# Optimization experiments

Measured on AMD Instinct MI355X. Metric: run time of the kernel, lower is better.

Reference implementation:

```python
import jax, jax.numpy as jnp
import numpy as np

LAMDA = 0.2  # config['lamda']
T, B, NI, IL, NS, H = 24, 64, 32, 24, 256, 256  # steps, batch, n_inputs, input_len(=vec), n_stations, hidden


def setup_inputs() -> dict:
    key = jax.random.key(0)
    ks = jax.random.split(key, 24)
    VEC, DIN = IL, NI + NS
    n = lambda k, s, sc=1.0: jax.random.normal(k, s, dtype=jnp.float32) * sc
    return {
        'local_inputs': n(ks[0], (T, B, NI)),
        'global_inputs': n(ks[1], (T, B, NS)),
        'local_states': n(ks[2], (B, NI, IL)),
        'global_states': n(ks[3], (B, NS, NI, IL)),
        'distmat': n(ks[4], (B, NS)),
        'local_attn0': jax.random.uniform(ks[5], (B, NI), jnp.float32, -0.25, 0.25),
        'global_attn0': jax.random.uniform(ks[6], (B, NS), jnp.float32, -0.15, 0.15),
        # conv_local_u: 1x1 conv over [B, IL, NI, 1] -> weight [VEC, IL]
        'Wcl': n(ks[7], (VEC, IL), 0.1), 'bcl': n(ks[8], (VEC,), 0.05),
        'Wll': n(ks[9], (VEC, H), 0.05), 'bll': n(ks[10], (VEC,), 0.05),
        'vl': n(ks[11], (VEC,)),
        # conv_global_k: kernel (1, NI) over [B, IL, NS, NI] -> weight [VEC, IL, NI]
        'Wcg': n(ks[12], (VEC, IL, NI), 0.05), 'bcg': n(ks[13], (VEC,), 0.05),
        'Wlg': n(ks[14], (VEC, H), 0.05), 'blg': n(ks[15], (VEC,), 0.05),
        'vg': n(ks[16], (VEC,)),
        # LSTM cell (called with zero h0/c0 every step, as in the source)
        'Wih': n(ks[17], (4 * H, DIN), 0.05),
        'bih': n(ks[18], (4 * H,), 0.05),
        'bhh': n(ks[19], (4 * H,), 0.05),
    }


def reference(local_inputs, global_inputs, local_states, global_states, distmat,
              local_attn0, global_attn0, Wcl, bcl, Wll, bll, vl,
              Wcg, bcg, Wlg, blg, vg, Wih, bih, bhh):
    b, ni, il = local_states.shape
    ns = global_states.shape[1]
    # raw .view() reshapes as in the torch code (NOT transposes)
    lhid = local_states.reshape(b, il, ni)                 # [B, IL, NI]
    hf_l = jnp.einsum('oc,bcl->bol', Wcl, lhid) + bcl[None, :, None]   # 1x1 conv
    ghid = global_states.reshape(b, il, ns, ni)            # [B, IL, NS, NI]
    hf_g = jnp.einsum('ocj,bcsj->bos', Wcg, ghid) + bcg[None, :, None]  # (1,NI) conv

    def step(carry, xs):
        la, ga = carry
        l_inp, g_inp = xs
        x = jnp.concatenate([la * l_inp, ga * g_inp], axis=1)  # [B, NI+NS]
        gates = x @ Wih.T + bih + bhh                          # h0 = 0 -> no Whh term
        i_g, f_g, g_g, o_g = jnp.split(gates, 4, axis=1)       # torch gate order i,f,g,o
        c = jax.nn.sigmoid(i_g) * jnp.tanh(g_g)                # c0 = 0 -> forget term drops
        h = jax.nn.sigmoid(o_g) * jnp.tanh(c)
        q = c                                                  # query = LSTM state
        y_l = q @ Wll.T + bll                                  # [B, VEC]
        s_l = jnp.einsum('bold,d->bl', jnp.tanh(hf_l[:, :, :, None] + y_l[:, None, None, :]), vl)
        la_n = jax.nn.softmax(s_l, axis=1)
        y_g = q @ Wlg.T + blg
        s_g = jnp.einsum('bosd,d->bs', jnp.tanh(hf_g[:, :, :, None] + y_g[:, None, None, :]), vg)
        s_g = (1.0 - LAMDA) * s_g + LAMDA * distmat
        ga_n = jax.nn.softmax(s_g, axis=1)
        return (la_n, ga_n), (h, c, la_n, ga_n)

    _, (outs, cs, las, gas) = jax.lax.scan(step, (local_attn0, global_attn0),
                                           (local_inputs, global_inputs))
    return outs, cs[-1], las, gas
```

## Files before the change

### kernel.cpp

```cpp
#include <hip/hip_runtime.h>

#define T_     24
#define LAMDA_ 0.2f

#define OFF_CS  393216
#define OFF_LAS 409600
#define OFF_GAS 458752

__device__ __forceinline__ float clamp15(float x){ return fminf(15.f, fmaxf(-15.f, x)); }
__device__ __forceinline__ float rcp_(float x){ return __builtin_amdgcn_rcpf(x); }

__global__ __launch_bounds__(1024, 4) void spat_kernel(
    const float* __restrict__ li,  const float* __restrict__ gi,
    const float* __restrict__ ls,  const float* __restrict__ gs,
    const float* __restrict__ dist,
    const float* __restrict__ la0, const float* __restrict__ ga0,
    const float* __restrict__ Wcl, const float* __restrict__ bcl,
    const float* __restrict__ Wll, const float* __restrict__ bll, const float* __restrict__ vl,
    const float* __restrict__ Wcg, const float* __restrict__ bcg,
    const float* __restrict__ Wlg, const float* __restrict__ blg, const float* __restrict__ vg,
    const float* __restrict__ Wih, const float* __restrict__ bih, const float* __restrict__ bhh,
    float* __restrict__ out)
{
    __shared__ float Eg[6144];
    __shared__ float El[800];
    __shared__ __align__(16) union {
        float wcg[6144];
        struct {
            float sgred[1024];
            float red[800];
            float gbuf[768];
            float xv[288];
            float cq[256];
        } p;
    } U;
    __shared__ float dstf[256];
    __shared__ float bsum[768];
    __shared__ float bcf[48];
    __shared__ __align__(8) float2 fvl[24], fvg[24];
    __shared__ float vlf[24], vgf[24], cbuf[2];
    __shared__ float ldspad[10240];

    const int b = blockIdx.x, tid = threadIdx.x;
    const int s = tid & 255, ogrp = tid >> 8;

    if (__builtin_expect((int)blockIdx.x == -1, 0)) {
        ldspad[tid] = bcg[0];
        out[0] = ldspad[tid ^ 1];
    }

    if (tid < 256) dstf[tid] = dist[b*256 + tid];
    if (tid < 24)  { vlf[tid] = vl[tid]; vgf[tid] = vg[tid]; }
    if (tid < 48)  bcf[tid] = (tid < 24) ? bll[tid] : blg[tid - 24];
    if (tid < 768) {
        const int wrow = tid + ((tid >= 256) ? 256 : 0);
        bsum[tid] = bih[wrow] + bhh[wrow];
    }
    if (tid == 0)  { float s1 = 0.f; for (int d = 0; d < 24; d++) s1 += vl[d]; cbuf[0] = s1; }
    if (tid == 1)  { float s1 = 0.f; for (int d = 0; d < 24; d++) s1 += vg[d]; cbuf[1] = s1; }

    float acc[6];
#pragma unroll
    for (int i = 0; i < 6; i++) acc[i] = bcg[ogrp*6 + i];

    for (int hc = 0; hc < 3; hc++) {
        for (int k = tid; k < 6144; k += 1024) {
            const int o = k >> 8, r = k & 255;
            U.wcg[k] = Wcg[o*768 + hc*256 + r];
        }
        __syncthreads();
        for (int cc = 0; cc < 8; cc++) {
            const int c = hc*8 + cc;
            const float4* gp = (const float4*)(gs + ((size_t)b*196608 + c*8192 + s*32));
#pragma unroll
            for (int h = 0; h < 2; h++) {
                float gv[16];
#pragma unroll
                for (int m = 0; m < 4; m++) {
                    const float4 g = gp[h*4 + m];
                    gv[4*m] = g.x; gv[4*m+1] = g.y; gv[4*m+2] = g.z; gv[4*m+3] = g.w;
                }
#pragma unroll
                for (int i = 0; i < 6; i++) {
                    const float4* wp = (const float4*)(U.wcg + ((ogrp*6 + i)*256 + cc*32)) + h*4;
                    float a = acc[i];
#pragma unroll
                    for (int m = 0; m < 4; m++) {
                        const float4 w = wp[m];
                        a = fmaf(w.x, gv[4*m],   a);
                        a = fmaf(w.y, gv[4*m+1], a);
                        a = fmaf(w.z, gv[4*m+2], a);
                        a = fmaf(w.w, gv[4*m+3], a);
                    }
                    acc[i] = a;
                }
            }
        }
        __syncthreads();
    }
#pragma unroll
    for (int i = 0; i < 6; i++) Eg[(ogrp*6 + i)*256 + s] = __expf(2.f*clamp15(acc[i]));

    if (tid < 768) {
        const int o = tid >> 5, l = tid & 31;
        float a = bcl[o];
        for (int c = 0; c < 24; c++)
            a = fmaf(Wcl[o*24 + c], ls[b*768 + c*32 + l], a);
        El[l*25 + o] = __expf(2.f*clamp15(a));
    }

    if (tid < 288) {
        if (tid < 32) U.p.xv[tid] = la0[b*32 + tid] * li[b*32 + tid];
        else { const int ss = tid - 32; U.p.xv[tid] = ga0[b*256 + ss] * gi[b*256 + ss]; }
    }
    __syncthreads();

    const int u8 = tid & 7, slot = tid >> 3;
    const int rbase = slot*6;

    for (int t = 0; t < T_; t++) {
        float liN = 0.f;
        float giN0 = 0.f, giN1 = 0.f, giN2 = 0.f, giN3 = 0.f;
        if (t < T_ - 1) {
            if (tid < 32) liN = li[(t+1)*2048 + b*32 + tid];
            else if (tid >= 64 && tid < 128) {
                const int lane = tid - 64;
                giN0 = gi[(t+1)*16384 + b*256 + lane];
                giN1 = gi[(t+1)*16384 + b*256 + lane + 64];
                giN2 = gi[(t+1)*16384 + b*256 + lane + 128];
                giN3 = gi[(t+1)*16384 + b*256 + lane + 192];
            }
        }

        {
            const float4* xp = (const float4*)U.p.xv;
            float ar0 = 0.f, ar1 = 0.f, ar2 = 0.f, ar3 = 0.f, ar4 = 0.f, ar5 = 0.f;
#pragma unroll 1
            for (int jc = 0; jc < 3; jc++) {
                const float4 x0 = xp[jc*24 + u8];
                const float4 x1 = xp[jc*24 + 8 + u8];
                const float4 x2 = xp[jc*24 + 16 + u8];

#define KROW(kk, AR) { \
                const int row_ = rbase + (kk); \
                const int wrow_ = row_ + ((row_ >= 256) ? 256 : 0); \
                const float4* wp_ = (const float4*)(Wih + wrow_*288) + jc*24 + u8; \
                const float4 w0_ = wp_[0], w1_ = wp_[8], w2_ = wp_[16]; \
                float a_ = AR; \
                a_ = fmaf(w0_.x,x0.x,a_); a_ = fmaf(w0_.y,x0.y,a_); \
                a_ = fmaf(w0_.z,x0.z,a_); a_ = fmaf(w0_.w,x0.w,a_); \
                a_ = fmaf(w1_.x,x1.x,a_); a_ = fmaf(w1_.y,x1.y,a_); \
                a_ = fmaf(w1_.z,x1.z,a_); a_ = fmaf(w1_.w,x1.w,a_); \
                a_ = fmaf(w2_.x,x2.x,a_); a_ = fmaf(w2_.y,x2.y,a_); \
                a_ = fmaf(w2_.z,x2.z,a_); a_ = fmaf(w2_.w,x2.w,a_); \
                AR = a_; }

                KROW(0, ar0) KROW(1, ar1)
                __builtin_amdgcn_sched_barrier(0);
                KROW(2, ar2) KROW(3, ar3)
                __builtin_amdgcn_sched_barrier(0);
                KROW(4, ar4) KROW(5, ar5)
                __builtin_amdgcn_sched_barrier(0);
#undef KROW
            }
            {
                float a_;
#define RED(kk, AR) { a_ = AR; \
                a_ += __shfl_xor(a_, 1); a_ += __shfl_xor(a_, 2); a_ += __shfl_xor(a_, 4); \
                if (u8 == 0) { const int row_ = rbase + (kk); U.p.gbuf[row_] = a_ + bsum[row_]; } }
                RED(0, ar0) RED(1, ar1) RED(2, ar2) RED(3, ar3) RED(4, ar4) RED(5, ar5)
#undef RED
            }
        }
        __syncthreads();

        if (tid < 256) {
            const float ig = U.p.gbuf[tid], gg = U.p.gbuf[256 + tid], ot = U.p.gbuf[512 + tid];
            const float sig_i = rcp_(1.f + __expf(-ig));
            const float th_g  = 1.f - 2.f*rcp_(1.f + __expf(2.f*clamp15(gg)));
            const float c     = sig_i * th_g;
            const float sig_o = rcp_(1.f + __expf(-ot));
            const float th_c  = 1.f - 2.f*rcp_(1.f + __expf(2.f*c));
            const float h     = sig_o * th_c;
            U.p.cq[tid] = c;
            out[t*16384 + b*256 + tid] = h;
            if (t == T_ - 1) out[OFF_CS + b*256 + tid] = c;
        }
        __syncthreads();

        if (tid < 384) {
            const int dot = slot;
            const float* Wr = (dot < 24) ? (Wll + dot*256) : (Wlg + (dot - 24)*256);
            const float4* wp = (const float4*)Wr;
            const float4* cp = (const float4*)U.p.cq;
            float a0 = 0.f, a1 = 0.f;
#pragma unroll
            for (int j = 0; j < 8; j += 2) {
                const float4 w0 = wp[j*8 + u8],     c0 = cp[j*8 + u8];
                const float4 w1 = wp[(j+1)*8 + u8], c1 = cp[(j+1)*8 + u8];
                a0 = fmaf(w0.x,c0.x,a0); a0 = fmaf(w0.y,c0.y,a0);
                a0 = fmaf(w0.z,c0.z,a0); a0 = fmaf(w0.w,c0.w,a0);
                a1 = fmaf(w1.x,c1.x,a1); a1 = fmaf(w1.y,c1.y,a1);
                a1 = fmaf(w1.z,c1.z,a1); a1 = fmaf(w1.w,c1.w,a1);
            }
            float a = a0 + a1;
            a += __shfl_xor(a, 1); a += __shfl_xor(a, 2); a += __shfl_xor(a, 4);
            if (u8 == 0) {
                const float F = __expf(2.f*clamp15(a + bcf[dot]));
                if (dot < 24) fvl[dot] = make_float2(F, vlf[dot]);
                else          fvg[dot - 24] = make_float2(F, vgf[dot - 24]);
            }
        }
        __syncthreads();

        {
            float Ew[6];
#pragma unroll
            for (int i = 0; i < 6; i++) Ew[i] = Eg[(ogrp*6 + i)*256 + s];
            float a0 = 0.f;
#pragma unroll
            for (int d = 0; d < 24; d++) {
                const float2 p = fvg[d];
                const float r0 = rcp_(fmaf(Ew[0], p.x, 1.f));
                const float r1 = rcp_(fmaf(Ew[1], p.x, 1.f));
                const float r2 = rcp_(fmaf(Ew[2], p.x, 1.f));
                const float r3 = rcp_(fmaf(Ew[3], p.x, 1.f));
                const float r4 = rcp_(fmaf(Ew[4], p.x, 1.f));
                const float r5 = rcp_(fmaf(Ew[5], p.x, 1.f));
                a0 = fmaf(p.y, ((r0 + r1) + (r2 + r3)) + (r4 + r5), a0);
            }
            U.p.sgred[tid] = a0;
        }
        if (tid < 768) {
            const int l = tid / 24, o = tid - l*24;
            const float E = El[l*25 + o];
            float b0 = 0.f, b1 = 0.f;
#pragma unroll
            for (int d = 0; d < 24; d += 2) {
                const float2 p0 = fvl[d], p1 = fvl[d+1];
                b0 = fmaf(p0.y, rcp_(fmaf(E, p0.x, 1.f)), b0);
                b1 = fmaf(p1.y, rcp_(fmaf(E, p1.x, 1.f)), b1);
            }
            U.p.red[l*25 + o] = b0 + b1;
        }
        __syncthreads();

        if (tid < 32) {
            float tot = 0.f;
#pragma unroll
            for (int o2 = 0; o2 < 24; o2++) tot += U.p.red[tid*25 + o2];
            const float sv = 24.f*cbuf[0] - 2.f*tot;
            float m = sv;
#pragma unroll
            for (int mk = 16; mk >= 1; mk >>= 1) m = fmaxf(m, __shfl_xor(m, mk));
            const float e = __expf(sv - m);
            float ss = e;
#pragma unroll
            for (int mk = 16; mk >= 1; mk >>= 1) ss += __shfl_xor(ss, mk);
            const float r = e * rcp_(ss);
            out[OFF_LAS + t*2048 + b*32 + tid] = r;
            if (t < T_ - 1) U.p.xv[tid] = r * liN;
        } else if (tid >= 64 && tid < 128) {
            const int lane = tid - 64;
            float vv0, vv1, vv2, vv3;
            {
                const float t0 = U.p.sgred[lane]     + U.p.sgred[256+lane]     + U.p.sgred[512+lane]     + U.p.sgred[768+lane];
                const float t1 = U.p.sgred[lane+64]  + U.p.sgred[256+lane+64]  + U.p.sgred[512+lane+64]  + U.p.sgred[768+lane+64];
                const float t2 = U.p.sgred[lane+128] + U.p.sgred[256+lane+128] + U.p.sgred[512+lane+128] + U.p.sgred[768+lane+128];
                const float t3 = U.p.sgred[lane+192] + U.p.sgred[256+lane+192] + U.p.sgred[512+lane+192] + U.p.sgred[768+lane+192];
                vv0 = (1.f-LAMDA_)*(24.f*cbuf[1] - 2.f*t0) + LAMDA_*dstf[lane];
                vv1 = (1.f-LAMDA_)*(24.f*cbuf[1] - 2.f*t1) + LAMDA_*dstf[lane+64];
                vv2 = (1.f-LAMDA_)*(24.f*cbuf[1] - 2.f*t2) + LAMDA_*dstf[lane+128];
                vv3 = (1.f-LAMDA_)*(24.f*cbuf[1] - 2.f*t3) + LAMDA_*dstf[lane+192];
            }
            float m = fmaxf(fmaxf(vv0, vv1), fmaxf(vv2, vv3));
#pragma unroll
            for (int mk = 32; mk >= 1; mk >>= 1) m = fmaxf(m, __shfl_xor(m, mk));
            const float e0 = __expf(vv0 - m), e1 = __expf(vv1 - m);
            const float e2 = __expf(vv2 - m), e3 = __expf(vv3 - m);
            float ss = (e0 + e1) + (e2 + e3);
#pragma unroll
            for (int mk = 32; mk >= 1; mk >>= 1) ss += __shfl_xor(ss, mk);
            const float inv = rcp_(ss);
            const float r0 = e0*inv, r1 = e1*inv, r2 = e2*inv, r3 = e3*inv;
            float* og = out + OFF_GAS + t*16384 + b*256;
            og[lane] = r0; og[lane+64] = r1; og[lane+128] = r2; og[lane+192] = r3;
            if (t < T_ - 1) {
                U.p.xv[32+lane]     = r0 * giN0;
                U.p.xv[32+lane+64]  = r1 * giN1;
                U.p.xv[32+lane+128] = r2 * giN2;
                U.p.xv[32+lane+192] = r3 * giN3;
            }
        }
        __syncthreads();
    }
}

extern "C" void kernel_launch(void* const* d_in, const int* in_sizes, int n_in,
                              void* d_out, int out_size, void* d_ws, size_t ws_size,
                              hipStream_t stream)
{
    const float* li   = (const float*)d_in[0];
    const float* gi   = (const float*)d_in[1];
    const float* ls   = (const float*)d_in[2];
    const float* gs   = (const float*)d_in[3];
    const float* dist = (const float*)d_in[4];
    const float* la0  = (const float*)d_in[5];
    const float* ga0  = (const float*)d_in[6];
    const float* Wcl  = (const float*)d_in[7];
    const float* bcl  = (const float*)d_in[8];
    const float* Wll  = (const float*)d_in[9];
    const float* bll  = (const float*)d_in[10];
    const float* vl   = (const float*)d_in[11];
    const float* Wcg  = (const float*)d_in[12];
    const float* bcg  = (const float*)d_in[13];
    const float* Wlg  = (const float*)d_in[14];
    const float* blg  = (const float*)d_in[15];
    const float* vg   = (const float*)d_in[16];
    const float* Wih  = (const float*)d_in[17];
    const float* bih  = (const float*)d_in[18];
    const float* bhh  = (const float*)d_in[19];

    spat_kernel<<<64, 1024, 0, stream>>>(li, gi, ls, gs, dist, la0, ga0,
                                         Wcl, bcl, Wll, bll, vl,
                                         Wcg, bcg, Wlg, blg, vg,
                                         Wih, bih, bhh, (float*)d_out);
}
```

Baseline: 542.5 us.

## Pair attention terms into rational form and buffer outputs in shared memory

Adjacent vector dimensions of the tanh-sum attention score are combined algebraically into one rational function per pair, with numerator and denominator coefficients precomputed. This halves the number of reciprocal operations in both the global and local attention loops. The local attention reduction now uses wave shuffles instead of a shared-memory array plus a serial sum. Per-step global output stores are buffered in shared memory and written out once after the time loop, and the padding LDS array is removed. Pairing changes rounding slightly and could lose precision when the E·F products are large.

```diff
diff --git a/kernel.cpp b/kernel.cpp
--- a/kernel.cpp
+++ b/kernel.cpp
@@ -24,30 +24,28 @@
 {
     __shared__ float Eg[6144];
     __shared__ float El[800];
+    __shared__ float outb[6144];
+    __shared__ float gasb[6144];
+    __shared__ float lasb[768];
+    __shared__ float csb[256];
     __shared__ __align__(16) union {
         float wcg[6144];
         struct {
             float sgred[1024];
-            float red[800];
             float gbuf[768];
             float xv[288];
             float cq[256];
+            float slg[32];
         } p;
     } U;
     __shared__ float dstf[256];
     __shared__ float bsum[768];
     __shared__ float bcf[48];
-    __shared__ __align__(8) float2 fvl[24], fvg[24];
+    __shared__ __align__(16) float4 pl4[12], pg4[12];
     __shared__ float vlf[24], vgf[24], cbuf[2];
-    __shared__ float ldspad[10240];
 
     const int b = blockIdx.x, tid = threadIdx.x;
     const int s = tid & 255, ogrp = tid >> 8;
-
-    if (__builtin_expect((int)blockIdx.x == -1, 0)) {
-        ldspad[tid] = bcg[0];
-        out[0] = ldspad[tid ^ 1];
-    }
 
     if (tid < 256) dstf[tid] = dist[b*256 + tid];
     if (tid < 24)  { vlf[tid] = vl[tid]; vgf[tid] = vg[tid]; }
@@ -117,6 +115,7 @@
 
     const int u8 = tid & 7, slot = tid >> 3;
     const int rbase = slot*6;
+    const int lg = tid >> 5, ol = tid & 31;
 
     for (int t = 0; t < T_; t++) {
         float liN = 0.f;
@@ -155,11 +154,9 @@
                 a_ = fmaf(w2_.z,x2.z,a_); a_ = fmaf(w2_.w,x2.w,a_); \
                 AR = a_; }
 
-                KROW(0, ar0) KROW(1, ar1)
+                KROW(0, ar0) KROW(1, ar1) KROW(2, ar2)
                 __builtin_amdgcn_sched_barrier(0);
-                KROW(2, ar2) KROW(3, ar3)
-                __builtin_amdgcn_sched_barrier(0);
-                KROW(4, ar4) KROW(5, ar5)
+                KROW(3, ar3) KROW(4, ar4) KROW(5, ar5)
                 __builtin_amdgcn_sched_barrier(0);
 #undef KROW
             }
@@ -183,8 +180,8 @@
             const float th_c  = 1.f - 2.f*rcp_(1.f + __expf(2.f*c));
             const float h     = sig_o * th_c;
             U.p.cq[tid] = c;
-            out[t*16384 + b*256 + tid] = h;
-            if (t == T_ - 1) out[OFF_CS + b*256 + tid] = c;
+            outb[t*256 + tid] = h;
+            if (t == T_ - 1) csb[tid] = c;
         }
         __syncthreads();
 
@@ -205,51 +202,64 @@
             }
             float a = a0 + a1;
             a += __shfl_xor(a, 1); a += __shfl_xor(a, 2); a += __shfl_xor(a, 4);
-            if (u8 == 0) {
-                const float F = __expf(2.f*clamp15(a + bcf[dot]));
-                if (dot < 24) fvl[dot] = make_float2(F, vlf[dot]);
-                else          fvg[dot - 24] = make_float2(F, vgf[dot - 24]);
+            const float F  = __expf(2.f*clamp15(a + bcf[dot]));
+            const float v  = (dot < 24) ? vlf[dot] : vgf[dot - 24];
+            const float Fo = __shfl_xor(F, 8);
+            const float vo = (dot < 24) ? vlf[dot ^ 1] : vgf[(dot ^ 1) - 24];
+            if ((tid & 15) == 0) {
+                const float A0 = v + vo;
+                const float A1 = fmaf(v, Fo, vo * F);
+                const float B1 = F + Fo;
+                const float B2 = F * Fo;
+                const int P = slot >> 1;
+                if (P < 12) pl4[P]      = make_float4(A0, A1, B1, B2);
+                else        pg4[P - 12] = make_float4(A0, A1, B1, B2);
             }
         }
         __syncthreads();
 
         {
-            float Ew[6];
-#pragma unroll
-            for (int i = 0; i < 6; i++) Ew[i] = Eg[(ogrp*6 + i)*256 + s];
+            float z[6], z2[6];
+#pragma unroll
+            for (int i = 0; i < 6; i++) {
+                z[i]  = Eg[(ogrp*6 + i)*256 + s];
+                z2[i] = z[i]*z[i];
+            }
             float a0 = 0.f;
-#pragma unroll
-            for (int d = 0; d < 24; d++) {
-                const float2 p = fvg[d];
-                const float r0 = rcp_(fmaf(Ew[0], p.x, 1.f));
-                const float r1 = rcp_(fmaf(Ew[1], p.x, 1.f));
-                const float r2 = rcp_(fmaf(Ew[2], p.x, 1.f));
-                const float r3 = rcp_(fmaf(Ew[3], p.x, 1.f));
-                const float r4 = rcp_(fmaf(Ew[4], p.x, 1.f));
-                const float r5 = rcp_(fmaf(Ew[5], p.x, 1.f));
-                a0 = fmaf(p.y, ((r0 + r1) + (r2 + r3)) + (r4 + r5), a0);
+#pragma unroll 4
+            for (int p = 0; p < 12; p++) {
+                const float4 q = pg4[p];
+#pragma unroll
+                for (int i = 0; i < 6; i++) {
+                    const float num = fmaf(z[i],  q.y, q.x);
+                    const float den = fmaf(z2[i], q.w, fmaf(z[i], q.z, 1.f));
+                    a0 = fmaf(num, rcp_(den), a0);
+                }
             }
             U.p.sgred[tid] = a0;
         }
-        if (tid < 768) {
-            const int l = tid / 24, o = tid - l*24;
-            const float E = El[l*25 + o];
-            float b0 = 0.f, b1 = 0.f;
-#pragma unroll
-            for (int d = 0; d < 24; d += 2) {
-                const float2 p0 = fvl[d], p1 = fvl[d+1];
-                b0 = fmaf(p0.y, rcp_(fmaf(E, p0.x, 1.f)), b0);
-                b1 = fmaf(p1.y, rcp_(fmaf(E, p1.x, 1.f)), b1);
-            }
-            U.p.red[l*25 + o] = b0 + b1;
+        {
+            float bsl = 0.f;
+            if (ol < 24) {
+                const float E  = El[lg*25 + ol];
+                const float E2 = E*E;
+#pragma unroll 4
+                for (int p = 0; p < 12; p++) {
+                    const float4 q = pl4[p];
+                    const float num = fmaf(E,  q.y, q.x);
+                    const float den = fmaf(E2, q.w, fmaf(E, q.z, 1.f));
+                    bsl = fmaf(num, rcp_(den), bsl);
+                }
+            }
+            bsl += __shfl_xor(bsl, 1);  bsl += __shfl_xor(bsl, 2);
+            bsl += __shfl_xor(bsl, 4);  bsl += __shfl_xor(bsl, 8);
+            bsl += __shfl_xor(bsl, 16);
+            if (ol == 0) U.p.slg[lg] = bsl;
         }
         __syncthreads();
 
         if (tid < 32) {
-            float tot = 0.f;
-#pragma unroll
-            for (int o2 = 0; o2 < 24; o2++) tot += U.p.red[tid*25 + o2];
-            const float sv = 24.f*cbuf[0] - 2.f*tot;
+            const float sv = 24.f*cbuf[0] - 2.f*U.p.slg[tid];
             float m = sv;
 #pragma unroll
             for (int mk = 16; mk >= 1; mk >>= 1) m = fmaxf(m, __shfl_xor(m, mk));
@@ -258,7 +268,7 @@
 #pragma unroll
             for (int mk = 16; mk >= 1; mk >>= 1) ss += __shfl_xor(ss, mk);
             const float r = e * rcp_(ss);
-            out[OFF_LAS + t*2048 + b*32 + tid] = r;
+            lasb[t*32 + tid] = r;
             if (t < T_ - 1) U.p.xv[tid] = r * liN;
         } else if (tid >= 64 && tid < 128) {
             const int lane = tid - 64;
@@ -283,8 +293,8 @@
             for (int mk = 32; mk >= 1; mk >>= 1) ss += __shfl_xor(ss, mk);
             const float inv = rcp_(ss);
             const float r0 = e0*inv, r1 = e1*inv, r2 = e2*inv, r3 = e3*inv;
-            float* og = out + OFF_GAS + t*16384 + b*256;
-            og[lane] = r0; og[lane+64] = r1; og[lane+128] = r2; og[lane+192] = r3;
+            float* gb = gasb + t*256;
+            gb[lane] = r0; gb[lane+64] = r1; gb[lane+128] = r2; gb[lane+192] = r3;
             if (t < T_ - 1) {
                 U.p.xv[32+lane]     = r0 * giN0;
                 U.p.xv[32+lane+64]  = r1 * giN1;
@@ -294,6 +304,14 @@
         }
         __syncthreads();
     }
+
+    for (int k = tid; k < 6144; k += 1024) {
+        const int tt = k >> 8, ii = k & 255;
+        out[tt*16384 + b*256 + ii]           = outb[k];
+        out[OFF_GAS + tt*16384 + b*256 + ii] = gasb[k];
+    }
+    if (tid < 768) out[OFF_LAS + (tid >> 5)*2048 + b*32 + (tid & 31)] = lasb[tid];
+    if (tid < 256) out[OFF_CS + b*256 + tid] = csb[tid];
 }
 
 extern "C" void kernel_launch(void* const* d_in, const int* in_sizes, int n_in,
```

Measured after the change: 506.2 us. 1.07x faster.
